# Kernel tuning notes

Hardware: AMD Instinct MI355X
Metric: run time of the kernel (lower is better)

## Reference

```python
import jax, jax.numpy as jnp
import numpy as np

# pywt 'db4' decomposition low-pass filter (L = 8 taps)
_DEC_LO = np.array([
    -0.010597401784997278, 0.032883011666982945, 0.030841381835986965,
    -0.18703481171888114, -0.02798376941698385, 0.6308807679295904,
    0.7148465705525415, 0.23037781330885523], dtype=np.float32)
# pywt convention: dec_hi[n] = (-1)^(n+1) * dec_lo[L-1-n]
_SIGNS = np.array([-1.0, 1.0] * 4, dtype=np.float32)
_DEC_HI = _DEC_LO[::-1].copy() * _SIGNS

DEC_LO = jnp.asarray(_DEC_LO)
DEC_HI = jnp.asarray(_DEC_HI)
LEVELS = 3


def _dwt_per(x):
    """One level of periodization-mode DWT along axis 1.

    x: (B, N, F) with N even. Returns (cA, cD), each (B, N//2, F).
    Matches pywt: c[k] = sum_j f[j] * x[(2k + 1 - j) mod N].
    """
    N = x.shape[1]
    L = DEC_LO.shape[0]
    k = jnp.arange(N // 2)
    j = jnp.arange(L)
    idx = (2 * k[:, None] + 1 - j[None, :]) % N          # (N//2, L)
    g = x[:, idx, :]                                      # (B, N//2, L, F)
    cA = jnp.einsum('bklf,l->bkf', g, DEC_LO)
    cD = jnp.einsum('bklf,l->bkf', g, DEC_HI)
    return cA, cD


def reference(x):
    """Multilevel db4 wavedec (periodization) along axis -2 of (B, N, F).

    Returns the flat coefficient tensor (B, K, F) with pywt ordering
    [cA_L, cD_L, cD_{L-1}, ..., cD_1] concatenated along axis 1.
    """
    a = x
    details = []
    for _ in range(LEVELS):
        a, d = _dwt_per(a)
        details.append(d)
    return jnp.concatenate([a] + details[::-1], axis=1)


def setup_inputs() -> dict:
    key = jax.random.key(0)
    x = jax.random.normal(key, (64, 4096, 64), dtype=jnp.float32)
    return {"x": x}


if __name__ == "__main__":
    out = reference(**setup_inputs())
    print(out.shape)
```

## Files before the change

### kernel.cpp

```cpp
#include <hip/hip_runtime.h>


__device__ __forceinline__ float2 ld2(const float* p) {
    return *reinterpret_cast<const float2*>(p);
}
__device__ __forceinline__ void st2(float* p, float2 v) {
    *reinterpret_cast<float2*>(p) = v;
}
__device__ __forceinline__ float2 fma2(float2 a, float s, float2 c) {
    c.x = fmaf(a.x, s, c.x);
    c.y = fmaf(a.y, s, c.y);
    return c;
}

__global__ __launch_bounds__(256) void dwt3_fused_v2(
    const float* __restrict__ in,
    float* __restrict__ out)
{
    const float LOR[8] = { 0.23037781330885523f,   0.7148465705525415f,
                           0.6308807679295904f,   -0.02798376941698385f,
                          -0.18703481171888114f,   0.030841381835986965f,
                           0.032883011666982945f, -0.010597401784997278f};
    const float HIR[8] = {-0.010597401784997278f, -0.032883011666982945f,
                           0.030841381835986965f,  0.18703481171888114f,
                          -0.02798376941698385f,  -0.6308807679295904f,
                           0.7148465705525415f,   -0.23037781330885523f};

    const int bid  = blockIdx.x;
    const int swz  = (bid & 7) * 64 + (bid >> 3);

    const int lane = threadIdx.x & 63;
    const int wv   = threadIdx.x >> 6;
    const int f    = (lane & 31) * 2;
    const int tsub = lane >> 5;
    const int b    = swz >> 3;
    const int tile = (swz & 7) * 8 + wv * 2 + tsub;
    const int K3   = tile * 8;

    const float* inB  = in  + (size_t)b * 4096 * 64 + f;
    float*       outB = out + (size_t)b * 4096 * 64 + f;

    const int i1s = 4 * K3 - 18;

    float2 w0[8];
    float2 w1[8];
    float2 w2[8];
    #pragma unroll
    for (int m = 0; m < 8; ++m) {
        w1[m] = make_float2(0.f, 0.f);
        w2[m] = make_float2(0.f, 0.f);
    }

    #pragma unroll
    for (int m = 0; m < 8; ++m) {
        const int r = (2 * i1s - 6 + m) & 4095;
        w0[m] = ld2(inB + (size_t)r * 64);
    }

    #pragma unroll
    for (int s = 0; s < 50; ++s) {
        const int i1 = i1s + s;
        if (s > 0) {
            #pragma unroll
            for (int m = 0; m < 6; ++m) w0[m] = w0[m + 2];
            const int ra = (2 * i1)     & 4095;
            const int rb = (2 * i1 + 1) & 4095;
            w0[6] = ld2(inB + (size_t)ra * 64);
            w0[7] = ld2(inB + (size_t)rb * 64);
        }

        float2 a1 = make_float2(0.f, 0.f);
        #pragma unroll
        for (int m = 0; m < 8; ++m) a1 = fma2(w0[m], LOR[m], a1);
        if (s >= 18) {
            float2 d1 = make_float2(0.f, 0.f);
            #pragma unroll
            for (int m = 0; m < 8; ++m) d1 = fma2(w0[m], HIR[m], d1);
            st2(outB + (size_t)((2048 + i1) & 4095) * 64, d1);
        }
        #pragma unroll
        for (int m = 0; m < 7; ++m) w1[m] = w1[m + 1];
        w1[7] = a1;

        if ((s & 1) && s >= 7) {
            const int i2 = 2 * K3 + (s - 19) / 2;
            float2 a2 = make_float2(0.f, 0.f);
            #pragma unroll
            for (int m = 0; m < 8; ++m) a2 = fma2(w1[m], LOR[m], a2);
            if (s >= 19) {
                float2 d2 = make_float2(0.f, 0.f);
                #pragma unroll
                for (int m = 0; m < 8; ++m) d2 = fma2(w1[m], HIR[m], d2);
                st2(outB + (size_t)((1024 + i2) & 4095) * 64, d2);
            }
            #pragma unroll
            for (int m = 0; m < 7; ++m) w2[m] = w2[m + 1];
            w2[7] = a2;

            if (s >= 21 && ((s - 21) & 3) == 0) {
                const int i3 = K3 + (s - 21) / 4;
                float2 a3 = make_float2(0.f, 0.f);
                float2 d3 = make_float2(0.f, 0.f);
                #pragma unroll
                for (int m = 0; m < 8; ++m) {
                    a3 = fma2(w2[m], LOR[m], a3);
                    d3 = fma2(w2[m], HIR[m], d3);
                }
                st2(outB + (size_t)(i3 & 4095) * 64,         a3);
                st2(outB + (size_t)((512 + i3) & 4095) * 64, d3);
            }
        }
    }
}

extern "C" void kernel_launch(void* const* d_in, const int* in_sizes, int n_in,
                              void* d_out, int out_size, void* d_ws, size_t ws_size,
                              hipStream_t stream) {
    (void)in_sizes; (void)n_in; (void)out_size; (void)d_ws; (void)ws_size;
    const float* x = (const float*)d_in[0];
    float* out = (float*)d_out;
    dwt3_fused_v2<<<512, 256, 0, stream>>>(x, out);
}
```

Measured before the change: 115.7 us.

## Software-pipeline input loads in 16-row register chunks ahead of compute

Replaces the per-step pair of global loads with rotating 16-row register buffers that are issued two chunks ahead of use, so each thread keeps several loads in flight while computing. It also adds a launch-bounds minimum of 2 blocks per CU. The aim is to hide global memory latency in this memory-bound fused three-level DWT. The cost is much higher register pressure (about 58 float2 buffers), which could cause spills or lower occupancy.

```diff
diff --git a/kernel.cpp b/kernel.cpp
--- a/kernel.cpp
+++ b/kernel.cpp
@@ -13,7 +13,7 @@
     return c;
 }
 
-__global__ __launch_bounds__(256) void dwt3_fused_v2(
+__global__ __launch_bounds__(256, 2) void dwt3_fused_v4(
     const float* __restrict__ in,
     float* __restrict__ out)
 {
@@ -40,77 +40,112 @@
     const float* inB  = in  + (size_t)b * 4096 * 64 + f;
     float*       outB = out + (size_t)b * 4096 * 64 + f;
 
-    const int i1s = 4 * K3 - 18;
+    const int i1s   = 4 * K3 - 18;
+    const int tbase = 2 * i1s - 6;
 
-    float2 w0[8];
-    float2 w1[8];
-    float2 w2[8];
+    float2 bufA[16], bufB[16], bufC[16], bufD[10];
+
+    #define ISSUE(BUF, C, N)                                                  \
+        _Pragma("unroll")                                                     \
+        for (int j = 0; j < (N); ++j) {                                       \
+            BUF[j] = ld2(inB + (size_t)((tbase + 16 * (C) + j) & 4095) * 64); \
+        }
+
+    ISSUE(bufA, 0, 16)
+    ISSUE(bufB, 1, 16)
+    ISSUE(bufC, 2, 16)
+
+    float2 w0[8], w1[8], w2[8];
     #pragma unroll
     for (int m = 0; m < 8; ++m) {
         w1[m] = make_float2(0.f, 0.f);
         w2[m] = make_float2(0.f, 0.f);
     }
+    #pragma unroll
+    for (int m = 0; m < 8; ++m) w0[m] = bufA[m];
 
-    #pragma unroll
-    for (int m = 0; m < 8; ++m) {
-        const int r = (2 * i1s - 6 + m) & 4095;
-        w0[m] = ld2(inB + (size_t)r * 64);
+    #define STEP(S, X0, X1) {                                                  \
+        const int i1 = i1s + (S);                                              \
+        _Pragma("unroll")                                                      \
+        for (int m = 0; m < 6; ++m) w0[m] = w0[m + 2];                         \
+        w0[6] = (X0); w0[7] = (X1);                                            \
+        float2 a1 = make_float2(0.f, 0.f);                                     \
+        _Pragma("unroll")                                                      \
+        for (int m = 0; m < 8; ++m) a1 = fma2(w0[m], LOR[m], a1);              \
+        if ((S) >= 18) {                                                       \
+            float2 d1 = make_float2(0.f, 0.f);                                 \
+            _Pragma("unroll")                                                  \
+            for (int m = 0; m < 8; ++m) d1 = fma2(w0[m], HIR[m], d1);          \
+            st2(outB + (size_t)((2048 + i1) & 4095) * 64, d1);                 \
+        }                                                                      \
+        _Pragma("unroll")                                                      \
+        for (int m = 0; m < 7; ++m) w1[m] = w1[m + 1];                         \
+        w1[7] = a1;                                                            \
+        if (((S) & 1) && (S) >= 7) {                                           \
+            const int i2 = 2 * K3 + ((S) - 19) / 2;                            \
+            float2 a2 = make_float2(0.f, 0.f);                                 \
+            _Pragma("unroll")                                                  \
+            for (int m = 0; m < 8; ++m) a2 = fma2(w1[m], LOR[m], a2);          \
+            if ((S) >= 19) {                                                   \
+                float2 d2 = make_float2(0.f, 0.f);                             \
+                _Pragma("unroll")                                              \
+                for (int m = 0; m < 8; ++m) d2 = fma2(w1[m], HIR[m], d2);      \
+                st2(outB + (size_t)((1024 + i2) & 4095) * 64, d2);             \
+            }                                                                  \
+            _Pragma("unroll")                                                  \
+            for (int m = 0; m < 7; ++m) w2[m] = w2[m + 1];                     \
+            w2[7] = a2;                                                        \
+            if ((S) >= 21 && (((S) - 21) & 3) == 0) {                          \
+                const int i3 = K3 + ((S) - 21) / 4;                            \
+                float2 a3 = make_float2(0.f, 0.f);                             \
+                float2 d3 = make_float2(0.f, 0.f);                             \
+                _Pragma("unroll")                                              \
+                for (int m = 0; m < 8; ++m) {                                  \
+                    a3 = fma2(w2[m], LOR[m], a3);                              \
+                    d3 = fma2(w2[m], HIR[m], d3);                              \
+                }                                                              \
+                st2(outB + (size_t)(i3 & 4095) * 64,         a3);              \
+                st2(outB + (size_t)((512 + i3) & 4095) * 64, d3);              \
+            }                                                                  \
+        }                                                                      \
+    }
+
+    {
+        float2 a1 = make_float2(0.f, 0.f);
+        #pragma unroll
+        for (int m = 0; m < 8; ++m) a1 = fma2(w0[m], LOR[m], a1);
+        #pragma unroll
+        for (int m = 0; m < 7; ++m) w1[m] = w1[m + 1];
+        w1[7] = a1;
     }
 
     #pragma unroll
-    for (int s = 0; s < 50; ++s) {
-        const int i1 = i1s + s;
-        if (s > 0) {
-            #pragma unroll
-            for (int m = 0; m < 6; ++m) w0[m] = w0[m + 2];
-            const int ra = (2 * i1)     & 4095;
-            const int rb = (2 * i1 + 1) & 4095;
-            w0[6] = ld2(inB + (size_t)ra * 64);
-            w0[7] = ld2(inB + (size_t)rb * 64);
-        }
+    for (int s = 1; s <= 4; ++s) STEP(s, bufA[2 * s + 6], bufA[2 * s + 7])
 
-        float2 a1 = make_float2(0.f, 0.f);
-        #pragma unroll
-        for (int m = 0; m < 8; ++m) a1 = fma2(w0[m], LOR[m], a1);
-        if (s >= 18) {
-            float2 d1 = make_float2(0.f, 0.f);
-            #pragma unroll
-            for (int m = 0; m < 8; ++m) d1 = fma2(w0[m], HIR[m], d1);
-            st2(outB + (size_t)((2048 + i1) & 4095) * 64, d1);
-        }
-        #pragma unroll
-        for (int m = 0; m < 7; ++m) w1[m] = w1[m + 1];
-        w1[7] = a1;
+    ISSUE(bufA, 3, 16)
+    #pragma unroll
+    for (int s = 5; s <= 12; ++s) STEP(s, bufB[2 * s + 6 - 16], bufB[2 * s + 7 - 16])
 
-        if ((s & 1) && s >= 7) {
-            const int i2 = 2 * K3 + (s - 19) / 2;
-            float2 a2 = make_float2(0.f, 0.f);
-            #pragma unroll
-            for (int m = 0; m < 8; ++m) a2 = fma2(w1[m], LOR[m], a2);
-            if (s >= 19) {
-                float2 d2 = make_float2(0.f, 0.f);
-                #pragma unroll
-                for (int m = 0; m < 8; ++m) d2 = fma2(w1[m], HIR[m], d2);
-                st2(outB + (size_t)((1024 + i2) & 4095) * 64, d2);
-            }
-            #pragma unroll
-            for (int m = 0; m < 7; ++m) w2[m] = w2[m + 1];
-            w2[7] = a2;
+    ISSUE(bufB, 4, 16)
+    #pragma unroll
+    for (int s = 13; s <= 20; ++s) STEP(s, bufC[2 * s + 6 - 32], bufC[2 * s + 7 - 32])
 
-            if (s >= 21 && ((s - 21) & 3) == 0) {
-                const int i3 = K3 + (s - 21) / 4;
-                float2 a3 = make_float2(0.f, 0.f);
-                float2 d3 = make_float2(0.f, 0.f);
-                #pragma unroll
-                for (int m = 0; m < 8; ++m) {
-                    a3 = fma2(w2[m], LOR[m], a3);
-                    d3 = fma2(w2[m], HIR[m], d3);
-                }
-                st2(outB + (size_t)(i3 & 4095) * 64,         a3);
-                st2(outB + (size_t)((512 + i3) & 4095) * 64, d3);
-            }
-        }
-    }
+    ISSUE(bufC, 5, 16)
+    #pragma unroll
+    for (int s = 21; s <= 28; ++s) STEP(s, bufA[2 * s + 6 - 48], bufA[2 * s + 7 - 48])
+
+    ISSUE(bufD, 6, 10)
+    #pragma unroll
+    for (int s = 29; s <= 36; ++s) STEP(s, bufB[2 * s + 6 - 64], bufB[2 * s + 7 - 64])
+
+    #pragma unroll
+    for (int s = 37; s <= 44; ++s) STEP(s, bufC[2 * s + 6 - 80], bufC[2 * s + 7 - 80])
+
+    #pragma unroll
+    for (int s = 45; s <= 49; ++s) STEP(s, bufD[2 * s + 6 - 96], bufD[2 * s + 7 - 96])
+
+    #undef STEP
+    #undef ISSUE
 }
 
 extern "C" void kernel_launch(void* const* d_in, const int* in_sizes, int n_in,
@@ -119,5 +154,5 @@
     (void)in_sizes; (void)n_in; (void)out_size; (void)d_ws; (void)ws_size;
     const float* x = (const float*)d_in[0];
     float* out = (float*)d_out;
-    dwt3_fused_v2<<<512, 256, 0, stream>>>(x, out);
+    dwt3_fused_v4<<<512, 256, 0, stream>>>(x, out);
 }
```

Measured after the change: 117.2 us. About the same (+1.3%).
